# Kernel optimization log

Hardware: AMD Instinct MI355X
Metric: run time of the kernel (lower is better)

Reference implementation:

```python
import jax, jax.numpy as jnp
import numpy as np

CDIM = 32
SCALES = (1, 16, 64, 256, 1024, 4096)  # last entry == T
INV_TEMP = 100.0
ENT_W = 0.1
COMMIT_W = 0.2
Q_SCALE = 1.0 / float(np.sqrt(CDIM))


def _interp_area(x, pt):
    # x: [B, T, C] -> [B, pt, C]; T divisible by pt so 'area' == block mean
    B, T, C = x.shape
    return x.reshape(B, pt, T // pt, C).mean(axis=2)


def _interp_linear(x, T):
    # x: [B, pt, C] -> [B, T, C]; mode='linear', align_corners=False
    pt = x.shape[1]
    pos = (jnp.arange(T, dtype=jnp.float32) + 0.5) * (pt / T) - 0.5
    pos = jnp.clip(pos, 0.0, pt - 1.0)
    lo = jnp.floor(pos).astype(jnp.int32)
    hi = jnp.minimum(lo + 1, pt - 1)
    w = (pos - lo.astype(jnp.float32))[None, :, None]
    return x[:, lo] * (1.0 - w) + x[:, hi] * w


def _bsq(f):
    # L2 normalize (torch F.normalize: clamp_min on norm)
    f = f / jnp.maximum(jnp.linalg.norm(f, axis=-1, keepdims=True), 1e-12)
    # sign quantize with STE
    zhat = jnp.where(f > 0, Q_SCALE, -Q_SCALE).astype(f.dtype)
    quantized = f + jax.lax.stop_gradient(zhat - f)
    # soft entropy loss
    p = jax.nn.sigmoid(-4.0 * f * (INV_TEMP / float(np.sqrt(CDIM))))
    prob = jnp.stack([p, 1.0 - p], axis=-1)  # [B, T, C, 2]
    ent = lambda c: -(c * jnp.log(c + 1e-8)).sum(axis=-1)
    per_sample_entropy = ent(prob).sum(axis=-1).mean()
    avg_prob = prob.mean(axis=(0, 1))  # [C, 2]
    cb_entropy = ent(avg_prob).sum()
    entropy_penalty = (per_sample_entropy - cb_entropy) / INV_TEMP
    commit = ((jax.lax.stop_gradient(quantized) - f) ** 2).sum(axis=-1).mean()
    aux = entropy_penalty * ENT_W + commit * COMMIT_W
    bits = (quantized > 0).astype(jnp.int32)
    return quantized, bits, aux


def setup_inputs() -> dict:
    key = jax.random.key(0)
    B, T, C = 128, SCALES[-1], CDIM
    return {"f_BTC": jax.random.normal(key, (B, T, C), dtype=jnp.float32)}


def reference(f_BTC):
    B, T, C = f_BTC.shape
    quantized_out = jnp.zeros_like(f_BTC)
    residual = f_BTC
    losses, bit_list = [], []
    for pt in SCALES:
        interp_res = _interp_area(residual, pt) if pt != T else residual
        q, bits, loss = _bsq(interp_res)
        q = _interp_linear(q, T) if pt != T else q
        residual = residual - jax.lax.stop_gradient(q)
        quantized_out = quantized_out + q
        bit_list.append(bits)
        losses.append(loss)
    all_losses = jnp.stack(losses, axis=-1)       # [num_scales]
    all_bits = jnp.concatenate(bit_list, axis=1)  # [B, sum(SCALES), C]
    return quantized_out, all_bits, all_losses
```

## Files before the change

kernel.cpp:

```cpp
#include <hip/hip_runtime.h>
#include <hip/hip_bf16.h>
#include <cstddef>
#include <cstdint>

#define NB 128
#define NT 4096
#define NC 32
#define BITROWS 5457
#define CQ_ROWS 337
#define QOUT_ELEMS (NB*NT*NC)
#define BITS_ELEMS (NB*BITROWS*NC)

#define ACC_OFF  5521408
#define S16_OFF  5523456

__device__ __constant__ float kQSC = 0.17677669529663687f;
__device__ __constant__ float kSIG = 17.67766952966369f;

__device__ __forceinline__ float interp_eval(const float* __restrict__ q, int P, int t, int c) {
  float pos = ((float)t + 0.5f) * ((float)P * (1.0f / 4096.0f)) - 0.5f;
  pos = fminf(fmaxf(pos, 0.0f), (float)(P - 1));
  const int lo = (int)pos;
  const int hi = min(lo + 1, P - 1);
  const float w = pos - (float)lo;
  const float a = __fmul_rn(q[lo * NC + c], 1.0f - w);
  const float b = __fmul_rn(q[hi * NC + c], w);
  return __fadd_rn(a, b);
}

__device__ __forceinline__ float interp_evalS(const float* __restrict__ qbase, int sb, int P,
                                              float scale, int t, int c) {
  float pos = ((float)t + 0.5f) * scale - 0.5f;
  pos = fminf(fmaxf(pos, 0.0f), (float)(P - 1));
  const int lo = (int)pos;
  const int hi = min(lo + 1, P - 1);
  const float w = pos - (float)lo;
  const float a = __fmul_rn(qbase[(lo - sb) * NC + c], 1.0f - w);
  const float b = __fmul_rn(qbase[(hi - sb) * NC + c], w);
  return __fadd_rn(a, b);
}

__device__ __forceinline__ void quant_core(float m, float& qvv, float& fn, bool& bit) {
  float ss = m * m;
  #pragma unroll
  for (int mk = 16; mk; mk >>= 1) ss += __shfl_xor(ss, mk, 32);
  const float den = fmaxf(sqrtf(ss), 1e-12f);
  fn = m / den;
  bit = fn > 0.0f;
  const float zh = bit ? kQSC : -kQSC;
  qvv = fn + (zh - fn);
}

__device__ __forceinline__ void loss_piece(float fn, float qvv, float& p, float& ent, float& c2) {
  const float arg = (-4.0f * fn) * kSIG;
  p = __builtin_amdgcn_rcpf(1.0f + __expf(-arg));
  ent = -(p * __logf(p + 1e-8f) + (1.0f - p) * __logf((1.0f - p) + 1e-8f));
  const float d = qvv - fn;
  c2 = d * d;
}

__device__ __forceinline__ void process_elem(
    float msum, float invn, int b, int rowOff, int j, int c,
    float* qlsRow, float* __restrict__ qvG, float* __restrict__ bitsG,
    float& entA, float& comA, float& pA)
{
  const float m = msum * invn;
  float qvv, fn; bool bit;
  quant_core(m, qvv, fn, bit);
  if (qlsRow) qlsRow[c] = qvv;
  qvG[(size_t)b * (CQ_ROWS * NC) + (size_t)(rowOff + j) * NC + c] = qvv;
  bitsG[(size_t)b * (BITROWS * NC) + (size_t)(rowOff + j) * NC + c] = bit ? 1.0f : 0.0f;
  float p, ent, c2;
  loss_piece(fn, qvv, p, ent, c2);
  entA += ent; comA += c2; pA += p;
}

__device__ __forceinline__ void reduce_losses(
    int sIdx, float entA, float comA, float pA, int tid, int nWaves,
    double* __restrict__ acc, float* redE, float* redC, float* redP)
{
  float e = entA, cm = comA;
  #pragma unroll
  for (int mk = 32; mk; mk >>= 1) { e += __shfl_xor(e, mk, 64); cm += __shfl_xor(cm, mk, 64); }
  const float p = pA + __shfl_xor(pA, 32, 64);
  const int w = tid >> 6, lane = tid & 63;
  if (lane == 0) { redE[w] = e; redC[w] = cm; }
  if (lane < 32) redP[w * 32 + lane] = p;
  __syncthreads();
  if (tid == 0) {
    double te = 0.0, tc = 0.0;
    for (int i = 0; i < nWaves; ++i) { te += (double)redE[i]; tc += (double)redC[i]; }
    atomicAdd(&acc[sIdx], te);
    atomicAdd(&acc[6 + sIdx], tc);
  }
  if (tid < 32) {
    float tp = 0.0f;
    for (int i = 0; i < nWaves; ++i) tp += redP[i * 32 + tid];
    atomicAdd(&acc[12 + sIdx * 32 + tid], (double)tp);
  }
  __syncthreads();
}

__global__ __launch_bounds__(256) void k_sum16(const float4* __restrict__ f4, float4* __restrict__ S4) {
  const int idx = blockIdx.x * 256 + threadIdx.x;
  const int c4 = idx & 7;
  const int j  = (idx >> 3) & 255;
  const int b  = idx >> 11;
  const float4* p = f4 + (size_t)b * 32768 + (size_t)j * 128 + c4;
  float4 s = {0.f, 0.f, 0.f, 0.f};
  #pragma unroll
  for (int k = 0; k < 16; ++k) {
    const float4 v = p[k * 8];
    s.x += v.x; s.y += v.y; s.z += v.z; s.w += v.w;
  }
  S4[idx] = s;
}

__global__ __launch_bounds__(1024) void k_coarse(
    const float* __restrict__ S16g, float* __restrict__ qv,
    float* __restrict__ bitsOut, double* __restrict__ acc)
{
  __shared__ float S[256 * NC];
  __shared__ float qls[81 * NC];
  __shared__ float red[1024];
  __shared__ float redE[16], redC[16], redP[16 * 32];
  const int b = blockIdx.x, tid = threadIdx.x;
  const int c = tid & 31;

  for (int e = tid; e < 256 * NC; e += 1024) S[e] = S16g[(size_t)b * 8192 + e];
  __syncthreads();

  float entA, comA, pA;

  entA = comA = pA = 0.0f;
  {
    const int g = tid >> 5;
    float part = 0.0f;
    #pragma unroll
    for (int j = 0; j < 8; ++j) part += S[(g * 8 + j) * NC + c];
    red[tid] = part;
  }
  __syncthreads();
  if (tid < 32) {
    float msum = 0.0f;
    for (int g = 0; g < 32; ++g) msum += red[g * 32 + tid];
    process_elem(msum, 1.0f / 4096.0f, b, 0, 0, tid, &qls[0], qv, bitsOut, entA, comA, pA);
  }
  reduce_losses(0, entA, comA, pA, tid, 16, acc, redE, redC, redP);
  {
    const float corr = 16.0f * qls[c];
    for (int e = tid; e < 8192; e += 1024) S[e] -= corr;
  }
  __syncthreads();

  entA = comA = pA = 0.0f;
  if (tid < 512) {
    const int j = tid >> 5;
    float msum = 0.0f;
    for (int jj = 0; jj < 16; ++jj) msum += S[(j * 16 + jj) * NC + c];
    process_elem(msum, 1.0f / 256.0f, b, 1, j, c, &qls[(1 + j) * NC], qv, bitsOut, entA, comA, pA);
  }
  reduce_losses(1, entA, comA, pA, tid, 16, acc, redE, redC, redP);
  for (int e = tid; e < 8192; e += 1024) {
    const int jj = e >> 5;
    float cs = 0.0f;
    #pragma unroll
    for (int k = 0; k < 16; ++k) cs += interp_eval(&qls[1 * NC], 16, jj * 16 + k, c);
    S[e] -= cs;
  }
  __syncthreads();

  entA = comA = pA = 0.0f;
  for (int out = tid; out < 2048; out += 1024) {
    const int j = out >> 5;
    float msum = 0.0f;
    #pragma unroll
    for (int jj = 0; jj < 4; ++jj) msum += S[(j * 4 + jj) * NC + c];
    process_elem(msum, 1.0f / 64.0f, b, 17, j, c, &qls[(17 + j) * NC], qv, bitsOut, entA, comA, pA);
  }
  reduce_losses(2, entA, comA, pA, tid, 16, acc, redE, redC, redP);
  for (int e = tid; e < 8192; e += 1024) {
    const int jj = e >> 5;
    float cs = 0.0f;
    #pragma unroll
    for (int k = 0; k < 16; ++k) cs += interp_eval(&qls[17 * NC], 64, jj * 16 + k, c);
    S[e] -= cs;
  }
  __syncthreads();

  entA = comA = pA = 0.0f;
  for (int out = tid; out < 8192; out += 1024) {
    const int j = out >> 5;
    process_elem(S[out], 1.0f / 16.0f, b, 81, j, c, nullptr, qv, bitsOut, entA, comA, pA);
  }
  reduce_losses(3, entA, comA, pA, tid, 16, acc, redE, redC, redP);
}

__global__ __launch_bounds__(256) void k_fused(
    const float* __restrict__ f, const float* __restrict__ qv,
    float* __restrict__ qout, float* __restrict__ bitsOut, double* __restrict__ acc)
{
  __shared__ float qsl[33 * NC];
  __shared__ float rp[136 * NC];
  __shared__ float qpre[128 * NC];
  __shared__ float q4r[34 * NC];
  __shared__ float redE[4], redC[4], redP[4 * 32];

  const int b = blockIdx.x >> 5, seg = blockIdx.x & 31;
  const int t0 = seg << 7;
  const int tid = threadIdx.x, c = tid & 31, rloc = tid >> 5;
  const int R0 = max(t0 / 4 - 1, 0);
  const int R1 = min(t0 / 4 + 32, 1023);
  const int tb = R0 * 4, tn = (R1 - R0 + 1) * 4;
  const int S2B = min(max(t0 / 64 - 1, 0), 60);
  const int S3B = min(max(tb / 16 - 1, 0), 244);
  const size_t fb = (size_t)b * (NT * NC);
  const size_t bbits = (size_t)b * (BITROWS * NC);

  for (int e = tid; e < 33 * NC; e += 256) {
    const int r = e >> 5, cc = e & 31;
    int grow;
    if (e < 544)        grow = r;
    else if (e < 672)   grow = 17 + S2B + (r - 17);
    else                grow = 81 + S3B + (r - 21);
    qsl[e] = qv[(size_t)b * (CQ_ROWS * NC) + (size_t)grow * NC + cc];
  }
  __syncthreads();

  for (int pass = 0; pass < 17; ++pass) {
    const int tt = tb + pass * 8 + rloc;
    if (tt < tb + tn) {
      const float fv = f[fb + (size_t)tt * NC + c];
      float r = fv - qsl[c];
      r -= interp_evalS(qsl + 32,  0,   16,  0.00390625f, tt, c);
      r -= interp_evalS(qsl + 544, S2B, 64,  0.015625f,   tt, c);
      r -= interp_evalS(qsl + 672, S3B, 256, 0.0625f,     tt, c);
      rp[(tt - tb) * NC + c] = r;
      if (tt >= t0 && tt < t0 + 128) qpre[(tt - t0) * NC + c] = fv - r;
    }
  }
  __syncthreads();

  float entA = 0.f, comA = 0.f, pA = 0.f;
  for (int pass = 0; pass < 5; ++pass) {
    const int j = R0 + pass * 8 + rloc;
    if (j <= R1) {
      const int base = (4 * j - tb) * NC + c;
      const float msum = rp[base] + rp[base + NC] + rp[base + 2 * NC] + rp[base + 3 * NC];
      float qvv, fn; bool bit;
      quant_core(msum * 0.25f, qvv, fn, bit);
      q4r[(j - R0) * NC + c] = qvv;
      if (j >= t0 / 4 && j < t0 / 4 + 32) {
        bitsOut[bbits + (size_t)(337 + j) * NC + c] = bit ? 1.0f : 0.0f;
        float p, ent, c2;
        loss_piece(fn, qvv, p, ent, c2);
        entA += ent; comA += c2; pA += p;
      }
    }
  }
  reduce_losses(4, entA, comA, pA, tid, 4, acc, redE, redC, redP);

  entA = comA = pA = 0.f;
  for (int pass = 0; pass < 16; ++pass) {
    const int t = t0 + pass * 8 + rloc;
    const float rpv = rp[(t - tb) * NC + c];
    const float q4 = interp_evalS(q4r, R0, 1024, 0.25f, t, c);
    const float r = rpv - q4;
    float qvv, fn; bool bit;
    quant_core(r, qvv, fn, bit);
    qout[fb + (size_t)t * NC + c] = (qpre[(t - t0) * NC + c] + q4) + qvv;
    bitsOut[bbits + (size_t)(1361 + t) * NC + c] = bit ? 1.0f : 0.0f;
    float p, ent, c2;
    loss_piece(fn, qvv, p, ent, c2);
    entA += ent; comA += c2; pA += p;
  }
  reduce_losses(5, entA, comA, pA, tid, 4, acc, redE, redC, redP);
}

__global__ void k_losses(const double* __restrict__ acc, float* __restrict__ out) {
  const int s = threadIdx.x;
  if (s >= 6) return;
  const int pts[6] = {1, 16, 64, 256, 1024, 4096};
  const double n = 128.0 * (double)pts[s];
  const double pse = acc[s] / n;
  const double commit = acc[6 + s] / n;
  double cbe = 0.0;
  for (int c = 0; c < 32; ++c) {
    const double ap = acc[12 + s * 32 + c] / n;
    cbe += -(ap * log(ap + 1e-8) + (1.0 - ap) * log((1.0 - ap) + 1e-8));
  }
  const double pen = (pse - cbe) / 100.0;
  out[s] = (float)(pen * 0.1 + commit * 0.2);
}

extern "C" void kernel_launch(void* const* d_in, const int* in_sizes, int n_in,
                              void* d_out, int out_size, void* d_ws, size_t ws_size,
                              hipStream_t stream) {
  const float* f = (const float*)d_in[0];
  float* qout = (float*)d_out;
  float* bitsOut = qout + QOUT_ELEMS;
  float* lossesOut = qout + (QOUT_ELEMS + BITS_ELEMS);
  float* qv = (float*)d_ws;
  double* acc = (double*)((char*)d_ws + ACC_OFF);
  float* S16 = (float*)((char*)d_ws + S16_OFF);

  hipMemsetAsync(acc, 0, 204 * sizeof(double), stream);
  k_sum16<<<1024, 256, 0, stream>>>((const float4*)f, (float4*)S16);
  k_coarse<<<NB, 1024, 0, stream>>>(S16, qv, bitsOut, acc);
  k_fused<<<NB * 32, 256, 0, stream>>>(f, qv, qout, bitsOut, acc);
  k_losses<<<1, 64, 0, stream>>>(acc, lossesOut);
}
```

Baseline: 384.1 us.

## Move scale-64/256 quantization into per-segment fused blocks, shrink coarse kernel

```diff
diff --git a/kernel.cpp b/kernel.cpp
--- a/kernel.cpp
+++ b/kernel.cpp
@@ -7,26 +7,15 @@
 #define NT 4096
 #define NC 32
 #define BITROWS 5457
-#define CQ_ROWS 337
+#define S01_ROWS 17
 #define QOUT_ELEMS (NB*NT*NC)
 #define BITS_ELEMS (NB*BITROWS*NC)
 
-#define ACC_OFF  5521408
-#define S16_OFF  5523456
+#define ACC_OFF  278528
+#define S16_OFF  280160
 
 __device__ __constant__ float kQSC = 0.17677669529663687f;
 __device__ __constant__ float kSIG = 17.67766952966369f;
-
-__device__ __forceinline__ float interp_eval(const float* __restrict__ q, int P, int t, int c) {
-  float pos = ((float)t + 0.5f) * ((float)P * (1.0f / 4096.0f)) - 0.5f;
-  pos = fminf(fmaxf(pos, 0.0f), (float)(P - 1));
-  const int lo = (int)pos;
-  const int hi = min(lo + 1, P - 1);
-  const float w = pos - (float)lo;
-  const float a = __fmul_rn(q[lo * NC + c], 1.0f - w);
-  const float b = __fmul_rn(q[hi * NC + c], w);
-  return __fadd_rn(a, b);
-}
 
 __device__ __forceinline__ float interp_evalS(const float* __restrict__ qbase, int sb, int P,
                                               float scale, int t, int c) {
@@ -57,22 +46,6 @@
   ent = -(p * __logf(p + 1e-8f) + (1.0f - p) * __logf((1.0f - p) + 1e-8f));
   const float d = qvv - fn;
   c2 = d * d;
-}
-
-__device__ __forceinline__ void process_elem(
-    float msum, float invn, int b, int rowOff, int j, int c,
-    float* qlsRow, float* __restrict__ qvG, float* __restrict__ bitsG,
-    float& entA, float& comA, float& pA)
-{
-  const float m = msum * invn;
-  float qvv, fn; bool bit;
-  quant_core(m, qvv, fn, bit);
-  if (qlsRow) qlsRow[c] = qvv;
-  qvG[(size_t)b * (CQ_ROWS * NC) + (size_t)(rowOff + j) * NC + c] = qvv;
-  bitsG[(size_t)b * (BITROWS * NC) + (size_t)(rowOff + j) * NC + c] = bit ? 1.0f : 0.0f;
-  float p, ent, c2;
-  loss_piece(fn, qvv, p, ent, c2);
-  entA += ent; comA += c2; pA += p;
 }
 
 __device__ __forceinline__ void reduce_losses(
@@ -116,93 +89,67 @@
   S4[idx] = s;
 }
 
-__global__ __launch_bounds__(1024) void k_coarse(
+__global__ __launch_bounds__(1024) void k_s01(
     const float* __restrict__ S16g, float* __restrict__ qv,
     float* __restrict__ bitsOut, double* __restrict__ acc)
 {
-  __shared__ float S[256 * NC];
-  __shared__ float qls[81 * NC];
   __shared__ float red[1024];
+  __shared__ float q0s[NC];
   __shared__ float redE[16], redC[16], redP[16 * 32];
   const int b = blockIdx.x, tid = threadIdx.x;
-  const int c = tid & 31;
-
-  for (int e = tid; e < 256 * NC; e += 1024) S[e] = S16g[(size_t)b * 8192 + e];
-  __syncthreads();
-
-  float entA, comA, pA;
-
-  entA = comA = pA = 0.0f;
+  const int c = tid & 31, g = tid >> 5;
+  const size_t sb = (size_t)b * 8192;
+  const size_t qb = (size_t)b * (S01_ROWS * NC);
+  const size_t bb = (size_t)b * (BITROWS * NC);
+
+  float entA = 0.f, comA = 0.f, pA = 0.f;
   {
-    const int g = tid >> 5;
     float part = 0.0f;
     #pragma unroll
-    for (int j = 0; j < 8; ++j) part += S[(g * 8 + j) * NC + c];
+    for (int j = 0; j < 8; ++j) part += S16g[sb + (size_t)(g * 8 + j) * NC + c];
     red[tid] = part;
   }
   __syncthreads();
   if (tid < 32) {
     float msum = 0.0f;
-    for (int g = 0; g < 32; ++g) msum += red[g * 32 + tid];
-    process_elem(msum, 1.0f / 4096.0f, b, 0, 0, tid, &qls[0], qv, bitsOut, entA, comA, pA);
+    for (int g2 = 0; g2 < 32; ++g2) msum += red[g2 * 32 + tid];
+    float qvv, fn; bool bit;
+    quant_core(msum * (1.0f / 4096.0f), qvv, fn, bit);
+    q0s[tid] = qvv;
+    qv[qb + tid] = qvv;
+    bitsOut[bb + tid] = bit ? 1.0f : 0.0f;
+    float p, ent, c2; loss_piece(fn, qvv, p, ent, c2);
+    entA = ent; comA = c2; pA = p;
   }
   reduce_losses(0, entA, comA, pA, tid, 16, acc, redE, redC, redP);
-  {
-    const float corr = 16.0f * qls[c];
-    for (int e = tid; e < 8192; e += 1024) S[e] -= corr;
-  }
-  __syncthreads();
-
-  entA = comA = pA = 0.0f;
+
+  entA = comA = pA = 0.f;
+  const float corr = 16.0f * q0s[c];
   if (tid < 512) {
     const int j = tid >> 5;
     float msum = 0.0f;
-    for (int jj = 0; jj < 16; ++jj) msum += S[(j * 16 + jj) * NC + c];
-    process_elem(msum, 1.0f / 256.0f, b, 1, j, c, &qls[(1 + j) * NC], qv, bitsOut, entA, comA, pA);
+    for (int jj = 0; jj < 16; ++jj)
+      msum += (S16g[sb + (size_t)(j * 16 + jj) * NC + c] - corr);
+    float qvv, fn; bool bit;
+    quant_core(msum * (1.0f / 256.0f), qvv, fn, bit);
+    qv[qb + (size_t)(1 + j) * NC + c] = qvv;
+    bitsOut[bb + (size_t)(1 + j) * NC + c] = bit ? 1.0f : 0.0f;
+    float p, ent, c2; loss_piece(fn, qvv, p, ent, c2);
+    entA = ent; comA = c2; pA = p;
   }
   reduce_losses(1, entA, comA, pA, tid, 16, acc, redE, redC, redP);
-  for (int e = tid; e < 8192; e += 1024) {
-    const int jj = e >> 5;
-    float cs = 0.0f;
-    #pragma unroll
-    for (int k = 0; k < 16; ++k) cs += interp_eval(&qls[1 * NC], 16, jj * 16 + k, c);
-    S[e] -= cs;
-  }
-  __syncthreads();
-
-  entA = comA = pA = 0.0f;
-  for (int out = tid; out < 2048; out += 1024) {
-    const int j = out >> 5;
-    float msum = 0.0f;
-    #pragma unroll
-    for (int jj = 0; jj < 4; ++jj) msum += S[(j * 4 + jj) * NC + c];
-    process_elem(msum, 1.0f / 64.0f, b, 17, j, c, &qls[(17 + j) * NC], qv, bitsOut, entA, comA, pA);
-  }
-  reduce_losses(2, entA, comA, pA, tid, 16, acc, redE, redC, redP);
-  for (int e = tid; e < 8192; e += 1024) {
-    const int jj = e >> 5;
-    float cs = 0.0f;
-    #pragma unroll
-    for (int k = 0; k < 16; ++k) cs += interp_eval(&qls[17 * NC], 64, jj * 16 + k, c);
-    S[e] -= cs;
-  }
-  __syncthreads();
-
-  entA = comA = pA = 0.0f;
-  for (int out = tid; out < 8192; out += 1024) {
-    const int j = out >> 5;
-    process_elem(S[out], 1.0f / 16.0f, b, 81, j, c, nullptr, qv, bitsOut, entA, comA, pA);
-  }
-  reduce_losses(3, entA, comA, pA, tid, 16, acc, redE, redC, redP);
-}
-
-__global__ __launch_bounds__(256) void k_fused(
-    const float* __restrict__ f, const float* __restrict__ qv,
-    float* __restrict__ qout, float* __restrict__ bitsOut, double* __restrict__ acc)
+}
+
+__global__ __launch_bounds__(256, 8) void k_fused(
+    const float* __restrict__ f, const float* __restrict__ S16g,
+    const float* __restrict__ qv, float* __restrict__ qout,
+    float* __restrict__ bitsOut, double* __restrict__ acc)
 {
-  __shared__ float qsl[33 * NC];
+  __shared__ float qsl[S01_ROWS * NC];
+  __shared__ float Sres[16 * NC];
+  __shared__ float q2l[4 * NC];
+  __shared__ float q3l[12 * NC];
   __shared__ float rp[136 * NC];
-  __shared__ float qpre[128 * NC];
   __shared__ float q4r[34 * NC];
   __shared__ float redE[4], redC[4], redP[4 * 32];
 
@@ -210,41 +157,86 @@
   const int t0 = seg << 7;
   const int tid = threadIdx.x, c = tid & 31, rloc = tid >> 5;
   const int R0 = max(t0 / 4 - 1, 0);
-  const int R1 = min(t0 / 4 + 32, 1023);
-  const int tb = R0 * 4, tn = (R1 - R0 + 1) * 4;
+  const int R1v = min(t0 / 4 + 32, 1023);
+  const int tb = R0 * 4, tn = (R1v - R0 + 1) * 4;
   const int S2B = min(max(t0 / 64 - 1, 0), 60);
   const int S3B = min(max(tb / 16 - 1, 0), 244);
+  const int R16B = 4 * S2B;
   const size_t fb = (size_t)b * (NT * NC);
   const size_t bbits = (size_t)b * (BITROWS * NC);
 
-  for (int e = tid; e < 33 * NC; e += 256) {
-    const int r = e >> 5, cc = e & 31;
-    int grow;
-    if (e < 544)        grow = r;
-    else if (e < 672)   grow = 17 + S2B + (r - 17);
-    else                grow = 81 + S3B + (r - 21);
-    qsl[e] = qv[(size_t)b * (CQ_ROWS * NC) + (size_t)grow * NC + cc];
-  }
-  __syncthreads();
+  for (int e = tid; e < S01_ROWS * NC; e += 256)
+    qsl[e] = qv[(size_t)b * (S01_ROWS * NC) + e];
+  __syncthreads();
+
+  const float corr = 16.0f * qsl[c];
+  for (int e = tid; e < 16 * NC; e += 256) {
+    const int i = e >> 5;
+    const int r16 = R16B + i;
+    const float raw = S16g[(size_t)b * 8192 + (size_t)r16 * NC + c];
+    float cs = 0.0f;
+    #pragma unroll
+    for (int k = 0; k < 16; ++k)
+      cs += interp_evalS(qsl + NC, 0, 16, 0.00390625f, r16 * 16 + k, c);
+    Sres[e] = (raw - corr) - cs;
+  }
+  __syncthreads();
+
+  float entA = 0.f, comA = 0.f, pA = 0.f;
+  if (tid < 128) {
+    const int jj = tid >> 5;
+    const int j = S2B + jj;
+    const int base = (4 * jj) * NC + c;
+    const float msum = Sres[base] + Sres[base + NC] + Sres[base + 2 * NC] + Sres[base + 3 * NC];
+    float qvv, fn; bool bit;
+    quant_core(msum * (1.0f / 64.0f), qvv, fn, bit);
+    q2l[jj * NC + c] = qvv;
+    if (j >= (t0 >> 6) && j < (t0 >> 6) + 2) {
+      bitsOut[bbits + (size_t)(17 + j) * NC + c] = bit ? 1.0f : 0.0f;
+      float p, ent, c2; loss_piece(fn, qvv, p, ent, c2);
+      entA += ent; comA += c2; pA += p;
+    }
+  }
+  reduce_losses(2, entA, comA, pA, tid, 4, acc, redE, redC, redP);
+
+  entA = comA = pA = 0.f;
+  for (int e = tid; e < 12 * NC; e += 256) {
+    const int i2 = e >> 5;
+    const int j3 = S3B + i2;
+    const int iloc = j3 - R16B;
+    float cs = 0.0f;
+    #pragma unroll
+    for (int k = 0; k < 16; ++k)
+      cs += interp_evalS(q2l, S2B, 64, 0.015625f, j3 * 16 + k, c);
+    const float v = Sres[iloc * NC + c] - cs;
+    float qvv, fn; bool bit;
+    quant_core(v * 0.0625f, qvv, fn, bit);
+    q3l[i2 * NC + c] = qvv;
+    if (j3 >= (t0 >> 4) && j3 < (t0 >> 4) + 8) {
+      bitsOut[bbits + (size_t)(81 + j3) * NC + c] = bit ? 1.0f : 0.0f;
+      float p, ent, c2; loss_piece(fn, qvv, p, ent, c2);
+      entA += ent; comA += c2; pA += p;
+    }
+  }
+  reduce_losses(3, entA, comA, pA, tid, 4, acc, redE, redC, redP);
 
   for (int pass = 0; pass < 17; ++pass) {
     const int tt = tb + pass * 8 + rloc;
     if (tt < tb + tn) {
       const float fv = f[fb + (size_t)tt * NC + c];
       float r = fv - qsl[c];
-      r -= interp_evalS(qsl + 32,  0,   16,  0.00390625f, tt, c);
-      r -= interp_evalS(qsl + 544, S2B, 64,  0.015625f,   tt, c);
-      r -= interp_evalS(qsl + 672, S3B, 256, 0.0625f,     tt, c);
+      r -= interp_evalS(qsl + NC, 0,   16,  0.00390625f, tt, c);
+      r -= interp_evalS(q2l,      S2B, 64,  0.015625f,   tt, c);
+      r -= interp_evalS(q3l,      S3B, 256, 0.0625f,     tt, c);
       rp[(tt - tb) * NC + c] = r;
-      if (tt >= t0 && tt < t0 + 128) qpre[(tt - t0) * NC + c] = fv - r;
     }
   }
   __syncthreads();
 
-  float entA = 0.f, comA = 0.f, pA = 0.f;
+  entA = comA = pA = 0.f;
   for (int pass = 0; pass < 5; ++pass) {
     const int j = R0 + pass * 8 + rloc;
-    if (j <= R1) {
+    if (j <= R1v) {
       const int base = (4 * j - tb) * NC + c;
       const float msum = rp[base] + rp[base + NC] + rp[base + 2 * NC] + rp[base + 3 * NC];
       float qvv, fn; bool bit;
@@ -252,8 +244,7 @@
       q4r[(j - R0) * NC + c] = qvv;
       if (j >= t0 / 4 && j < t0 / 4 + 32) {
         bitsOut[bbits + (size_t)(337 + j) * NC + c] = bit ? 1.0f : 0.0f;
-        float p, ent, c2;
-        loss_piece(fn, qvv, p, ent, c2);
+        float p, ent, c2; loss_piece(fn, qvv, p, ent, c2);
         entA += ent; comA += c2; pA += p;
       }
     }
@@ -263,15 +254,16 @@
   entA = comA = pA = 0.f;
   for (int pass = 0; pass < 16; ++pass) {
     const int t = t0 + pass * 8 + rloc;
+    const float fv = f[fb + (size_t)t * NC + c];
     const float rpv = rp[(t - tb) * NC + c];
     const float q4 = interp_evalS(q4r, R0, 1024, 0.25f, t, c);
     const float r = rpv - q4;
     float qvv, fn; bool bit;
     quant_core(r, qvv, fn, bit);
-    qout[fb + (size_t)t * NC + c] = (qpre[(t - t0) * NC + c] + q4) + qvv;
+    const float qpre = fv - rpv;
+    qout[fb + (size_t)t * NC + c] = (qpre + q4) + qvv;
     bitsOut[bbits + (size_t)(1361 + t) * NC + c] = bit ? 1.0f : 0.0f;
-    float p, ent, c2;
-    loss_piece(fn, qvv, p, ent, c2);
+    float p, ent, c2; loss_piece(fn, qvv, p, ent, c2);
     entA += ent; comA += c2; pA += p;
   }
   reduce_losses(5, entA, comA, pA, tid, 4, acc, redE, redC, redP);
@@ -306,7 +298,7 @@
 
   hipMemsetAsync(acc, 0, 204 * sizeof(double), stream);
   k_sum16<<<1024, 256, 0, stream>>>((const float4*)f, (float4*)S16);
-  k_coarse<<<NB, 1024, 0, stream>>>(S16, qv, bitsOut, acc);
-  k_fused<<<NB * 32, 256, 0, stream>>>(f, qv, qout, bitsOut, acc);
+  k_s01<<<NB, 1024, 0, stream>>>(S16, qv, bitsOut, acc);
+  k_fused<<<NB * 32, 256, 0, stream>>>(f, S16, qv, qout, bitsOut, acc);
   k_losses<<<1, 64, 0, stream>>>(acc, lossesOut);
 }
```

After: 432.2 us. 12.5% more time.
